# Performance work log

Hardware: AMD Instinct MI355X
Metric: run time of the kernel (lower is better)

## Reference

```python
import jax, jax.numpy as jnp
import numpy as np

N_NODES = 100000
F_IN = 512
HIDDEN = 64
N_CLASS = 40
N_EDGES = 3200000


def gcn_conv(x, src, dst, deg_inv_sqrt, W, b, n_nodes):
    # PyG GCNConv: linear transform, then deg^{-1/2} A_hat deg^{-1/2} aggregation, then bias
    h = x @ W  # [N, out]
    norm = deg_inv_sqrt[src] * deg_inv_sqrt[dst]  # [E+N] (includes self-loops)
    msg = h[src] * norm[:, None]  # gather + scale
    out = jax.ops.segment_sum(msg, dst, num_segments=n_nodes)  # scatter-add
    return out + b


def setup_inputs() -> dict:
    key = jax.random.key(0)
    k1, k2, k3, k4, k5 = jax.random.split(key, 5)
    x = jax.random.normal(k1, (N_NODES, F_IN), dtype=jnp.float32)
    edge_index = jax.random.randint(k2, (2, N_EDGES), 0, N_NODES, dtype=jnp.int64)
    # Glorot-style init for GCN weights
    W1 = jax.random.normal(k3, (F_IN, HIDDEN), dtype=jnp.float32) / np.sqrt(F_IN)
    b1 = jnp.zeros((HIDDEN,), dtype=jnp.float32)
    W2 = jax.random.normal(k4, (HIDDEN, N_CLASS), dtype=jnp.float32) / np.sqrt(HIDDEN)
    b2 = jnp.zeros((N_CLASS,), dtype=jnp.float32)
    return {"x": x, "edge_index": edge_index, "W1": W1, "b1": b1, "W2": W2, "b2": b2}


def reference(x, edge_index, W1, b1, W2, b2):
    n = x.shape[0]
    loops = jnp.arange(n, dtype=edge_index.dtype)
    src = jnp.concatenate([edge_index[0], loops])  # add self-loops (GCNConv default)
    dst = jnp.concatenate([edge_index[1], loops])
    deg = jax.ops.segment_sum(jnp.ones_like(dst, dtype=x.dtype), dst, num_segments=n)
    deg_inv_sqrt = jnp.where(deg > 0, jax.lax.rsqrt(deg), 0.0)
    h = gcn_conv(x, src, dst, deg_inv_sqrt, W1, b1, n)
    h = jax.nn.relu(h)  # dropout treated as eval-mode identity
    x_out = gcn_conv(h, src, dst, deg_inv_sqrt, W2, b2, n)
    return jax.nn.log_softmax(x_out, axis=1), x_out
```

## Files before the change

### kernel.cpp

```cpp
#include <hip/hip_runtime.h>
#include <math.h>

#define N_NODES 100000
#define F_IN    512
#define HIDDEN  64
#define N_CLASS 40
#define N_EDGES 3200000
#define NB      782
#define CAP     6144
#define EPB     8192
#define NPB     391

typedef int EIdx;

typedef __attribute__((ext_vector_type(8))) short short8;
typedef __attribute__((ext_vector_type(4))) float f32x4;
typedef __attribute__((ext_vector_type(4))) unsigned uint4v;

__device__ inline short f2bf(float f) {
    unsigned u = __builtin_bit_cast(unsigned, f);
    unsigned r = u + 0x7FFFu + ((u >> 16) & 1u);
    return (short)(r >> 16);
}

__device__ inline unsigned cvtpk(float lo, float hi) {
    unsigned r;
    asm("v_cvt_pk_bf16_f32 %0, %1, %2" : "=v"(r) : "v"(lo), "v"(hi));
    return r;
}

__device__ inline float bflo(unsigned w) { return __builtin_bit_cast(float, w << 16); }
__device__ inline float bfhi(unsigned w) { return __builtin_bit_cast(float, w & 0xFFFF0000u); }

__global__ __launch_bounds__(256) void binit_kernel(int* __restrict__ bcur) {
    int i = blockIdx.x * 256 + threadIdx.x;
    if (i < NB) bcur[i] = i * CAP;
}

__global__ __launch_bounds__(256) void part1_kernel(const EIdx* __restrict__ src,
                                                    const EIdx* __restrict__ dst,
                                                    int* __restrict__ bcur,
                                                    unsigned* __restrict__ bpacked) {
    __shared__ int hist[NB];
    __shared__ int excl[NB];
    __shared__ int cur[NB];
    __shared__ int delta[NB];
    __shared__ int stmp[256];
    __shared__ unsigned spk[EPB];
    __shared__ unsigned short bid[EPB];
    int t = threadIdx.x;
    int e0 = blockIdx.x * EPB;
    int dreg[32];
    for (int j = t; j < NB; j += 256) hist[j] = 0;
    __syncthreads();
#pragma unroll
    for (int k = 0; k < 32; ++k) {
        int e = e0 + k * 256 + t;
        dreg[k] = (e < N_EDGES) ? dst[e] : -1;
        if (dreg[k] >= 0) atomicAdd(&hist[dreg[k] >> 7], 1);
    }
    __syncthreads();
    {
        int i0 = 4 * t;
        int v0 = (i0 < NB) ? hist[i0] : 0;
        int v1 = (i0 + 1 < NB) ? hist[i0 + 1] : 0;
        int v2 = (i0 + 2 < NB) ? hist[i0 + 2] : 0;
        int v3 = (i0 + 3 < NB) ? hist[i0 + 3] : 0;
        int s = v0 + v1 + v2 + v3;
        stmp[t] = s;
        __syncthreads();
        for (int o = 1; o < 256; o <<= 1) {
            int a = (t >= o) ? stmp[t - o] : 0;
            __syncthreads();
            stmp[t] += a;
            __syncthreads();
        }
        int E = stmp[t] - s;
        if (i0 < NB) excl[i0] = E;
        if (i0 + 1 < NB) excl[i0 + 1] = E + v0;
        if (i0 + 2 < NB) excl[i0 + 2] = E + v0 + v1;
        if (i0 + 3 < NB) excl[i0 + 3] = E + v0 + v1 + v2;
    }
    __syncthreads();
    for (int j = t; j < NB; j += 256) {
        int h = hist[j];
        int rsv = h ? atomicAdd(&bcur[j], h) : 0;
        delta[j] = rsv - excl[j];
        cur[j] = excl[j];
    }
    __syncthreads();
#pragma unroll
    for (int k = 0; k < 32; ++k) {
        int d = dreg[k];
        if (d >= 0) {
            int e = e0 + k * 256 + t;
            int s = src[e];
            int b = d >> 7;
            int p = atomicAdd(&cur[b], 1);
            spk[p] = ((unsigned)(d & 127) << 20) | (unsigned)s;
            bid[p] = (unsigned short)b;
        }
    }
    __syncthreads();
    int cnt = N_EDGES - e0;
    if (cnt > EPB) cnt = EPB;
    for (int i = t; i < cnt; i += 256) {
        int bb = bid[i];
        int pos = i + delta[bb];
        if (pos < (bb + 1) * CAP) bpacked[pos] = spk[i];
    }
}

__global__ __launch_bounds__(256) void part2_kernel(const int* __restrict__ bcur,
                                                    const unsigned* __restrict__ bpacked,
                                                    int* __restrict__ csr_src,
                                                    unsigned* __restrict__ rowmeta,
                                                    float* __restrict__ dis) {
    __shared__ unsigned ent[CAP];
    __shared__ int hist[128];
    __shared__ int stmp[128];
    __shared__ int cur[128];
    int t = threadIdx.x;
    int bk = blockIdx.x;
    int base = bk * CAP;
    int cnt = bcur[bk] - base;
    if (cnt > CAP) cnt = CAP;
    if (t < 128) hist[t] = 0;
    __syncthreads();
    for (int i = t; i < cnt; i += 256) {
        unsigned p = bpacked[base + i];
        ent[i] = p;
        atomicAdd(&hist[p >> 20], 1);
    }
    __syncthreads();
    if (t < 128) stmp[t] = hist[t];
    __syncthreads();
    for (int o = 1; o < 128; o <<= 1) {
        int a = (t >= o && t < 128) ? stmp[t - o] : 0;
        __syncthreads();
        if (t < 128) stmp[t] += a;
        __syncthreads();
    }
    if (t < 128) {
        int ex = stmp[t] - hist[t];
        cur[t] = ex;
        int n = (bk << 7) + t;
        if (n < N_NODES) {
            rowmeta[n] = (unsigned)(base + ex) | ((unsigned)hist[t] << 23);
            dis[n] = rsqrtf((float)(hist[t] + 1));
        }
    }
    __syncthreads();
    for (int i = t; i < cnt; i += 256) {
        unsigned p = ent[i];
        int p2 = atomicAdd(&cur[p >> 20], 1);
        csr_src[base + p2] = (int)(p & 0xFFFFFu);
    }
}

__global__ __launch_bounds__(256) void wprep_kernel(const float* __restrict__ W,
                                                    short* __restrict__ Wbf) {
    int idx = blockIdx.x * 256 + threadIdx.x;
    int k = idx >> 6, col = idx & 63;
    Wbf[col * F_IN + (k ^ ((col & 7) << 3))] = f2bf(W[idx]);
}

__global__ __launch_bounds__(256) void gemm1_mfma_kernel(const float* __restrict__ x,
                                                         const short* __restrict__ Wbf,
                                                         const float* __restrict__ dis,
                                                         unsigned* __restrict__ h1b) {
    __shared__ short Wt[HIDDEN * 128];
    __shared__ short xs[128 * 40];
    int tid = threadIdx.x;
    int wave = tid >> 6, lane = tid & 63;
    int r0 = blockIdx.x * 128;
    int wr0 = r0 + wave * 32;
    int lrow = lane & 15;
    int lk = (lane >> 4) * 8;
    int bswz = (lane & 7) << 3;

    f32x4 acc[2][4];
#pragma unroll
    for (int m = 0; m < 2; ++m)
#pragma unroll
        for (int n = 0; n < 4; ++n) acc[m][n] = (f32x4)0.0f;

    int srow = tid >> 3;
    int schunk = tid & 7;
    int grow[4];
#pragma unroll
    for (int i = 0; i < 4; ++i) {
        int r = r0 + srow + i * 32;
        grow[i] = (r < N_NODES) ? r : (N_NODES - 1);
    }

    float4 xr[4];
#pragma unroll
    for (int i = 0; i < 4; ++i)
        xr[i] = *reinterpret_cast<const float4*>(x + (size_t)grow[i] * F_IN + 4 * schunk);

    const short8* Wv = (const short8*)Wbf;
    short8* Lv = (short8*)Wt;

    for (int ks = 0; ks < 16; ++ks) {
        int kg = ks * 32;
        __syncthreads();
#pragma unroll
        for (int i = 0; i < 4; ++i) {
            uint2 u = {cvtpk(xr[i].x, xr[i].y), cvtpk(xr[i].z, xr[i].w)};
            *reinterpret_cast<uint2*>(&xs[(srow + i * 32) * 40 + 4 * schunk]) = u;
        }
        if ((kg & 127) == 0) {
            int q = kg >> 7;
            for (int i = tid; i < 1024; i += 256) {
                int col = i >> 4, kc = i & 15;
                Lv[i] = Wv[col * 64 + q * 16 + kc];
            }
        }
        __syncthreads();
        if (ks < 15) {
            int kn = kg + 32;
#pragma unroll
            for (int i = 0; i < 4; ++i)
                xr[i] = *reinterpret_cast<const float4*>(x + (size_t)grow[i] * F_IN + kn + 4 * schunk);
        }
        int k0loc = kg & 127;
        short8 a0 = *reinterpret_cast<const short8*>(&xs[(wave * 32 + lrow) * 40 + lk]);
        short8 a1 = *reinterpret_cast<const short8*>(&xs[(wave * 32 + 16 + lrow) * 40 + lk]);
        short8 b[4];
#pragma unroll
        for (int n = 0; n < 4; ++n) {
            int c = n * 16 + lrow;
            b[n] = *reinterpret_cast<const short8*>(&Wt[c * 128 + ((k0loc + lk) ^ bswz)]);
        }
#pragma unroll
        for (int n = 0; n < 4; ++n) {
            acc[0][n] = __builtin_amdgcn_mfma_f32_16x16x32_bf16(a0, b[n], acc[0][n], 0, 0, 0);
            acc[1][n] = __builtin_amdgcn_mfma_f32_16x16x32_bf16(a1, b[n], acc[1][n], 0, 0, 0);
        }
    }

    int crow = (lane >> 4) * 4, ccol = lane & 15;
    bool evenc = (ccol & 1) == 0;
#pragma unroll
    for (int m = 0; m < 2; ++m) {
#pragma unroll
        for (int j = 0; j < 4; ++j) {
            int rr = wr0 + m * 16 + crow + j;
            int rs = (rr < N_NODES) ? rr : (N_NODES - 1);
            float ds = dis[rs];
            float v[4], vn[4];
#pragma unroll
            for (int n = 0; n < 4; ++n) v[n] = acc[m][n][j] * ds;
#pragma unroll
            for (int n = 0; n < 4; ++n) vn[n] = __shfl_xor(v[n], 1);
            if (rr < N_NODES && evenc) {
#pragma unroll
                for (int n = 0; n < 4; ++n)
                    h1b[(size_t)rr * 32 + ((n * 16 + ccol) >> 1)] = cvtpk(v[n], vn[n]);
            }
        }
    }
}

__global__ __launch_bounds__(256) void gather1_kernel(const unsigned* __restrict__ h1b,
                                                      const unsigned* __restrict__ rowmeta,
                                                      const int* __restrict__ csr_src,
                                                      const float* __restrict__ dis,
                                                      const float* __restrict__ b1,
                                                      float* __restrict__ out) {
    int tid = threadIdx.x;
    int n = blockIdx.x * 32 + (tid >> 3);
    int l = tid & 7;
    unsigned meta = rowmeta[n];
    int base = (int)(meta & 0x7FFFFFu);
    int deg = (int)(meta >> 23);
    const unsigned* rowp = h1b + 4 * l;
    uint4 v = *reinterpret_cast<const uint4*>(h1b + (size_t)n * 32 + 4 * l);
    float a0 = bflo(v.x), a1 = bfhi(v.x), a2 = bflo(v.y), a3 = bfhi(v.y);
    float a4 = bflo(v.z), a5 = bfhi(v.z), a6 = bflo(v.w), a7 = bfhi(v.w);
    int e = 0;
    for (; e + 3 < deg; e += 4) {
        int s0 = csr_src[base + e],     s1 = csr_src[base + e + 1];
        int s2 = csr_src[base + e + 2], s3 = csr_src[base + e + 3];
        uint4 r0 = *reinterpret_cast<const uint4*>(rowp + (size_t)s0 * 32);
        uint4 r1 = *reinterpret_cast<const uint4*>(rowp + (size_t)s1 * 32);
        uint4 r2 = *reinterpret_cast<const uint4*>(rowp + (size_t)s2 * 32);
        uint4 r3 = *reinterpret_cast<const uint4*>(rowp + (size_t)s3 * 32);
        a0 += (bflo(r0.x) + bflo(r1.x)) + (bflo(r2.x) + bflo(r3.x));
        a1 += (bfhi(r0.x) + bfhi(r1.x)) + (bfhi(r2.x) + bfhi(r3.x));
        a2 += (bflo(r0.y) + bflo(r1.y)) + (bflo(r2.y) + bflo(r3.y));
        a3 += (bfhi(r0.y) + bfhi(r1.y)) + (bfhi(r2.y) + bfhi(r3.y));
        a4 += (bflo(r0.z) + bflo(r1.z)) + (bflo(r2.z) + bflo(r3.z));
        a5 += (bfhi(r0.z) + bfhi(r1.z)) + (bfhi(r2.z) + bfhi(r3.z));
        a6 += (bflo(r0.w) + bflo(r1.w)) + (bflo(r2.w) + bflo(r3.w));
        a7 += (bfhi(r0.w) + bfhi(r1.w)) + (bfhi(r2.w) + bfhi(r3.w));
    }
    for (; e < deg; ++e) {
        int s = csr_src[base + e];
        uint4 r = *reinterpret_cast<const uint4*>(rowp + (size_t)s * 32);
        a0 += bflo(r.x); a1 += bfhi(r.x); a2 += bflo(r.y); a3 += bfhi(r.y);
        a4 += bflo(r.z); a5 += bfhi(r.z); a6 += bflo(r.w); a7 += bfhi(r.w);
    }
    float ds = dis[n];
    float4 bL = *reinterpret_cast<const float4*>(b1 + 8 * l);
    float4 bH = *reinterpret_cast<const float4*>(b1 + 8 * l + 4);
    float4 oL = {fmaxf(fmaf(a0, ds, bL.x), 0.f), fmaxf(fmaf(a1, ds, bL.y), 0.f),
                 fmaxf(fmaf(a2, ds, bL.z), 0.f), fmaxf(fmaf(a3, ds, bL.w), 0.f)};
    float4 oH = {fmaxf(fmaf(a4, ds, bH.x), 0.f), fmaxf(fmaf(a5, ds, bH.y), 0.f),
                 fmaxf(fmaf(a6, ds, bH.z), 0.f), fmaxf(fmaf(a7, ds, bH.w), 0.f)};
    float* op = out + (size_t)n * HIDDEN + 8 * l;
    *reinterpret_cast<float4*>(op) = oL;
    *reinterpret_cast<float4*>(op + 4) = oH;
}

__global__ __launch_bounds__(256) void gemm2_kernel(const float* __restrict__ x,
                                                    const float* __restrict__ W,
                                                    const float* __restrict__ dis,
                                                    unsigned* __restrict__ h2b) {
    int r = blockIdx.x * 256 + threadIdx.x;
    if (r >= N_NODES) return;
    float acc[N_CLASS];
#pragma unroll
    for (int j = 0; j < N_CLASS; ++j) acc[j] = 0.0f;
    const float* xr = x + (size_t)r * HIDDEN;
    for (int k0 = 0; k0 < HIDDEN; k0 += 4) {
        float4 xv = *reinterpret_cast<const float4*>(xr + k0);
        const float* wk = W + (size_t)k0 * N_CLASS;
#pragma unroll
        for (int j = 0; j < N_CLASS; ++j) {
            acc[j] = fmaf(xv.x, wk[j], acc[j]);
            acc[j] = fmaf(xv.y, wk[N_CLASS + j], acc[j]);
            acc[j] = fmaf(xv.z, wk[2 * N_CLASS + j], acc[j]);
            acc[j] = fmaf(xv.w, wk[3 * N_CLASS + j], acc[j]);
        }
    }
    float ds = dis[r];
    unsigned* hr = h2b + (size_t)r * 20;
#pragma unroll
    for (int q = 0; q < 5; ++q) {
        uint4v o = {cvtpk(acc[8 * q] * ds,     acc[8 * q + 1] * ds),
                    cvtpk(acc[8 * q + 2] * ds, acc[8 * q + 3] * ds),
                    cvtpk(acc[8 * q + 4] * ds, acc[8 * q + 5] * ds),
                    cvtpk(acc[8 * q + 6] * ds, acc[8 * q + 7] * ds)};
        *reinterpret_cast<uint4v*>(hr + 4 * q) = o;
    }
}

__global__ __launch_bounds__(256) void gather2_kernel(const unsigned* __restrict__ h2b,
                                                      const unsigned* __restrict__ rowmeta,
                                                      const int* __restrict__ csr_src,
                                                      const float* __restrict__ dis,
                                                      const float* __restrict__ b2,
                                                      float* __restrict__ xout,
                                                      float* __restrict__ out_ls) {
    int tid = threadIdx.x;
    int n = blockIdx.x * 32 + (tid >> 3);
    int l = tid & 7;
    bool act = l < 5;
    unsigned meta = rowmeta[n];
    int base = (int)(meta & 0x7FFFFFu);
    int deg = (int)(meta >> 23);
    const unsigned* rowp = h2b + 4 * l;
    float a0 = 0.f, a1 = 0.f, a2 = 0.f, a3 = 0.f, a4 = 0.f, a5 = 0.f, a6 = 0.f, a7 = 0.f;
    if (act) {
        uint4 v = *reinterpret_cast<const uint4*>(h2b + (size_t)n * 20 + 4 * l);
        a0 = bflo(v.x); a1 = bfhi(v.x); a2 = bflo(v.y); a3 = bfhi(v.y);
        a4 = bflo(v.z); a5 = bfhi(v.z); a6 = bflo(v.w); a7 = bfhi(v.w);
    }
    int e = 0;
    for (; e + 3 < deg; e += 4) {
        int s0 = csr_src[base + e],     s1 = csr_src[base + e + 1];
        int s2 = csr_src[base + e + 2], s3 = csr_src[base + e + 3];
        if (act) {
            uint4 r0 = *reinterpret_cast<const uint4*>(rowp + (size_t)s0 * 20);
            uint4 r1 = *reinterpret_cast<const uint4*>(rowp + (size_t)s1 * 20);
            uint4 r2 = *reinterpret_cast<const uint4*>(rowp + (size_t)s2 * 20);
            uint4 r3 = *reinterpret_cast<const uint4*>(rowp + (size_t)s3 * 20);
            a0 += (bflo(r0.x) + bflo(r1.x)) + (bflo(r2.x) + bflo(r3.x));
            a1 += (bfhi(r0.x) + bfhi(r1.x)) + (bfhi(r2.x) + bfhi(r3.x));
            a2 += (bflo(r0.y) + bflo(r1.y)) + (bflo(r2.y) + bflo(r3.y));
            a3 += (bfhi(r0.y) + bfhi(r1.y)) + (bfhi(r2.y) + bfhi(r3.y));
            a4 += (bflo(r0.z) + bflo(r1.z)) + (bflo(r2.z) + bflo(r3.z));
            a5 += (bfhi(r0.z) + bfhi(r1.z)) + (bfhi(r2.z) + bfhi(r3.z));
            a6 += (bflo(r0.w) + bflo(r1.w)) + (bflo(r2.w) + bflo(r3.w));
            a7 += (bfhi(r0.w) + bfhi(r1.w)) + (bfhi(r2.w) + bfhi(r3.w));
        }
    }
    for (; e < deg; ++e) {
        int s = csr_src[base + e];
        if (act) {
            uint4 r = *reinterpret_cast<const uint4*>(rowp + (size_t)s * 20);
            a0 += bflo(r.x); a1 += bfhi(r.x); a2 += bflo(r.y); a3 += bfhi(r.y);
            a4 += bflo(r.z); a5 += bfhi(r.z); a6 += bflo(r.w); a7 += bfhi(r.w);
        }
    }
    float ds = dis[n];
    float v0 = 0.f, v1 = 0.f, v2 = 0.f, v3 = 0.f, v4 = 0.f, v5 = 0.f, v6 = 0.f, v7 = 0.f;
    if (act) {
        float4 bL = *reinterpret_cast<const float4*>(b2 + 8 * l);
        float4 bH = *reinterpret_cast<const float4*>(b2 + 8 * l + 4);
        v0 = fmaf(a0, ds, bL.x); v1 = fmaf(a1, ds, bL.y);
        v2 = fmaf(a2, ds, bL.z); v3 = fmaf(a3, ds, bL.w);
        v4 = fmaf(a4, ds, bH.x); v5 = fmaf(a5, ds, bH.y);
        v6 = fmaf(a6, ds, bH.z); v7 = fmaf(a7, ds, bH.w);
    }
    float mx = act ? fmaxf(fmaxf(fmaxf(v0, v1), fmaxf(v2, v3)),
                           fmaxf(fmaxf(v4, v5), fmaxf(v6, v7))) : -INFINITY;
    mx = fmaxf(mx, __shfl_xor(mx, 1));
    mx = fmaxf(mx, __shfl_xor(mx, 2));
    mx = fmaxf(mx, __shfl_xor(mx, 4));
    float sum = act ? ((expf(v0 - mx) + expf(v1 - mx)) + (expf(v2 - mx) + expf(v3 - mx))) +
                      ((expf(v4 - mx) + expf(v5 - mx)) + (expf(v6 - mx) + expf(v7 - mx))) : 0.f;
    sum += __shfl_xor(sum, 1);
    sum += __shfl_xor(sum, 2);
    sum += __shfl_xor(sum, 4);
    if (act) {
        float ls = mx + logf(sum);
        float* xp = xout + (size_t)n * N_CLASS + 8 * l;
        float* lp = out_ls + (size_t)n * N_CLASS + 8 * l;
        float4 xoL = {v0, v1, v2, v3};
        float4 xoH = {v4, v5, v6, v7};
        float4 loL = {v0 - ls, v1 - ls, v2 - ls, v3 - ls};
        float4 loH = {v4 - ls, v5 - ls, v6 - ls, v7 - ls};
        *reinterpret_cast<float4*>(xp) = xoL;
        *reinterpret_cast<float4*>(xp + 4) = xoH;
        *reinterpret_cast<float4*>(lp) = loL;
        *reinterpret_cast<float4*>(lp + 4) = loH;
    }
}

extern "C" void kernel_launch(void* const* d_in, const int* in_sizes, int n_in,
                              void* d_out, int out_size, void* d_ws, size_t ws_size,
                              hipStream_t stream) {
    const float* x  = (const float*)d_in[0];
    const EIdx*  ei = (const EIdx*)d_in[1];
    const float* W1 = (const float*)d_in[2];
    const float* b1 = (const float*)d_in[3];
    const float* W2 = (const float*)d_in[4];
    const float* b2 = (const float*)d_in[5];
    const EIdx* src = ei;
    const EIdx* dst = ei + N_EDGES;

    float* out_ls = (float*)d_out;
    float* x_out  = out_ls + (size_t)N_NODES * N_CLASS;

    char* w = (char*)d_ws;
    int*      bcur    = (int*)w;       w += 1024 * 4;
    float*    dis     = (float*)w;     w += 100352 * 4;
    unsigned* rowmeta = (unsigned*)w;  w += 100352 * 4;
    short*    Wbf     = (short*)w;     w += (size_t)F_IN * HIDDEN * 2;
    unsigned* bpacked = (unsigned*)w;
    unsigned* h1b     = (unsigned*)w;  w += (size_t)NB * CAP * 4;
    int*      csr_src = (int*)w;       w += (size_t)NB * CAP * 4;
    unsigned* h2b     = (unsigned*)w;  w += (size_t)N_NODES * 20 * 4;
    float*    agg1    = (float*)w;     w += (size_t)N_NODES * HIDDEN * 4;

    const int B = 256;
    int gG  = N_NODES / 32;
    int gN  = (N_NODES + B - 1) / B;
    int gM1 = (N_NODES + 127) / 128;

    binit_kernel<<<4, B, 0, stream>>>(bcur);
    part1_kernel<<<NPB, B, 0, stream>>>(src, dst, bcur, bpacked);
    part2_kernel<<<NB, B, 0, stream>>>(bcur, bpacked, csr_src, rowmeta, dis);
    wprep_kernel<<<(F_IN * HIDDEN) / B, B, 0, stream>>>(W1, Wbf);

    gemm1_mfma_kernel<<<gM1, B, 0, stream>>>(x, Wbf, dis, h1b);
    gather1_kernel<<<gG, B, 0, stream>>>(h1b, rowmeta, csr_src, dis, b1, agg1);

    gemm2_kernel<<<gN, B, 0, stream>>>(agg1, W2, dis, h2b);
    gather2_kernel<<<gG, B, 0, stream>>>(h2b, rowmeta, csr_src, dis, b2, x_out, out_ls);
}
```

Before: 273.5 us.

## Merge bucket init into wprep, split LDS histograms, widen gemm1 K-step

Measured after the change: 271.8 us. Within noise of the previous version (-0.6%).

```diff
diff --git a/kernel.cpp b/kernel.cpp
--- a/kernel.cpp
+++ b/kernel.cpp
@@ -32,40 +32,45 @@
 __device__ inline float bflo(unsigned w) { return __builtin_bit_cast(float, w << 16); }
 __device__ inline float bfhi(unsigned w) { return __builtin_bit_cast(float, w & 0xFFFF0000u); }
 
-__global__ __launch_bounds__(256) void binit_kernel(int* __restrict__ bcur) {
-    int i = blockIdx.x * 256 + threadIdx.x;
-    if (i < NB) bcur[i] = i * CAP;
+__global__ __launch_bounds__(256) void wprep_kernel(const float* __restrict__ W,
+                                                    short* __restrict__ Wbf,
+                                                    int* __restrict__ bcur) {
+    int idx = blockIdx.x * 256 + threadIdx.x;
+    if (idx < NB) bcur[idx] = idx * CAP;
+    int k = idx >> 6, col = idx & 63;
+    Wbf[col * F_IN + (k ^ ((col & 7) << 3))] = f2bf(W[idx]);
 }
 
 __global__ __launch_bounds__(256) void part1_kernel(const EIdx* __restrict__ src,
                                                     const EIdx* __restrict__ dst,
                                                     int* __restrict__ bcur,
                                                     unsigned* __restrict__ bpacked) {
-    __shared__ int hist[NB];
+    __shared__ int hist[2 * NB];
     __shared__ int excl[NB];
-    __shared__ int cur[NB];
+    __shared__ int cur[2 * NB];
     __shared__ int delta[NB];
     __shared__ int stmp[256];
     __shared__ unsigned spk[EPB];
     __shared__ unsigned short bid[EPB];
     int t = threadIdx.x;
+    int sub = t >> 7;
     int e0 = blockIdx.x * EPB;
     int dreg[32];
-    for (int j = t; j < NB; j += 256) hist[j] = 0;
+    for (int j = t; j < 2 * NB; j += 256) hist[j] = 0;
     __syncthreads();
 #pragma unroll
     for (int k = 0; k < 32; ++k) {
         int e = e0 + k * 256 + t;
         dreg[k] = (e < N_EDGES) ? dst[e] : -1;
-        if (dreg[k] >= 0) atomicAdd(&hist[dreg[k] >> 7], 1);
+        if (dreg[k] >= 0) atomicAdd(&hist[sub * NB + (dreg[k] >> 7)], 1);
     }
     __syncthreads();
     {
         int i0 = 4 * t;
-        int v0 = (i0 < NB) ? hist[i0] : 0;
-        int v1 = (i0 + 1 < NB) ? hist[i0 + 1] : 0;
-        int v2 = (i0 + 2 < NB) ? hist[i0 + 2] : 0;
-        int v3 = (i0 + 3 < NB) ? hist[i0 + 3] : 0;
+        int v0 = (i0 < NB) ? hist[i0] + hist[NB + i0] : 0;
+        int v1 = (i0 + 1 < NB) ? hist[i0 + 1] + hist[NB + i0 + 1] : 0;
+        int v2 = (i0 + 2 < NB) ? hist[i0 + 2] + hist[NB + i0 + 2] : 0;
+        int v3 = (i0 + 3 < NB) ? hist[i0 + 3] + hist[NB + i0 + 3] : 0;
         int s = v0 + v1 + v2 + v3;
         stmp[t] = s;
         __syncthreads();
@@ -83,10 +88,12 @@
     }
     __syncthreads();
     for (int j = t; j < NB; j += 256) {
-        int h = hist[j];
-        int rsv = h ? atomicAdd(&bcur[j], h) : 0;
+        int h0 = hist[j], h1 = hist[NB + j];
+        int tot = h0 + h1;
+        int rsv = tot ? atomicAdd(&bcur[j], tot) : 0;
         delta[j] = rsv - excl[j];
         cur[j] = excl[j];
+        cur[NB + j] = excl[j] + h0;
     }
     __syncthreads();
 #pragma unroll
@@ -96,7 +103,7 @@
             int e = e0 + k * 256 + t;
             int s = src[e];
             int b = d >> 7;
-            int p = atomicAdd(&cur[b], 1);
+            int p = atomicAdd(&cur[sub * NB + b], 1);
             spk[p] = ((unsigned)(d & 127) << 20) | (unsigned)s;
             bid[p] = (unsigned short)b;
         }
@@ -117,23 +124,24 @@
                                                     unsigned* __restrict__ rowmeta,
                                                     float* __restrict__ dis) {
     __shared__ unsigned ent[CAP];
-    __shared__ int hist[128];
+    __shared__ int hist[2 * 128];
     __shared__ int stmp[128];
-    __shared__ int cur[128];
+    __shared__ int cur[2 * 128];
     int t = threadIdx.x;
+    int sub = t >> 7;
     int bk = blockIdx.x;
     int base = bk * CAP;
     int cnt = bcur[bk] - base;
     if (cnt > CAP) cnt = CAP;
-    if (t < 128) hist[t] = 0;
+    hist[t] = 0;
     __syncthreads();
     for (int i = t; i < cnt; i += 256) {
         unsigned p = bpacked[base + i];
         ent[i] = p;
-        atomicAdd(&hist[p >> 20], 1);
-    }
-    __syncthreads();
-    if (t < 128) stmp[t] = hist[t];
+        atomicAdd(&hist[sub * 128 + (p >> 20)], 1);
+    }
+    __syncthreads();
+    if (t < 128) stmp[t] = hist[t] + hist[128 + t];
     __syncthreads();
     for (int o = 1; o < 128; o <<= 1) {
         int a = (t >= o && t < 128) ? stmp[t - o] : 0;
@@ -142,27 +150,22 @@
         __syncthreads();
     }
     if (t < 128) {
-        int ex = stmp[t] - hist[t];
+        int tot = hist[t] + hist[128 + t];
+        int ex = stmp[t] - tot;
         cur[t] = ex;
+        cur[128 + t] = ex + hist[t];
         int n = (bk << 7) + t;
         if (n < N_NODES) {
-            rowmeta[n] = (unsigned)(base + ex) | ((unsigned)hist[t] << 23);
-            dis[n] = rsqrtf((float)(hist[t] + 1));
+            rowmeta[n] = (unsigned)(base + ex) | ((unsigned)tot << 23);
+            dis[n] = rsqrtf((float)(tot + 1));
         }
     }
     __syncthreads();
     for (int i = t; i < cnt; i += 256) {
         unsigned p = ent[i];
-        int p2 = atomicAdd(&cur[p >> 20], 1);
+        int p2 = atomicAdd(&cur[sub * 128 + (p >> 20)], 1);
         csr_src[base + p2] = (int)(p & 0xFFFFFu);
     }
-}
-
-__global__ __launch_bounds__(256) void wprep_kernel(const float* __restrict__ W,
-                                                    short* __restrict__ Wbf) {
-    int idx = blockIdx.x * 256 + threadIdx.x;
-    int k = idx >> 6, col = idx & 63;
-    Wbf[col * F_IN + (k ^ ((col & 7) << 3))] = f2bf(W[idx]);
 }
 
 __global__ __launch_bounds__(256) void gemm1_mfma_kernel(const float* __restrict__ x,
@@ -170,7 +173,7 @@
                                                          const float* __restrict__ dis,
                                                          unsigned* __restrict__ h1b) {
     __shared__ short Wt[HIDDEN * 128];
-    __shared__ short xs[128 * 40];
+    __shared__ short xs[128 * 72];
     int tid = threadIdx.x;
     int wave = tid >> 6, lane = tid & 63;
     int r0 = blockIdx.x * 128;
@@ -185,58 +188,62 @@
 #pragma unroll
         for (int n = 0; n < 4; ++n) acc[m][n] = (f32x4)0.0f;
 
-    int srow = tid >> 3;
-    int schunk = tid & 7;
-    int grow[4];
-#pragma unroll
-    for (int i = 0; i < 4; ++i) {
-        int r = r0 + srow + i * 32;
+    int srow = tid >> 4;
+    int schunk = tid & 15;
+    int grow[8];
+#pragma unroll
+    for (int i = 0; i < 8; ++i) {
+        int r = r0 + srow + i * 16;
         grow[i] = (r < N_NODES) ? r : (N_NODES - 1);
     }
 
-    float4 xr[4];
-#pragma unroll
-    for (int i = 0; i < 4; ++i)
+    float4 xr[8];
+#pragma unroll
+    for (int i = 0; i < 8; ++i)
         xr[i] = *reinterpret_cast<const float4*>(x + (size_t)grow[i] * F_IN + 4 * schunk);
 
     const short8* Wv = (const short8*)Wbf;
     short8* Lv = (short8*)Wt;
 
-    for (int ks = 0; ks < 16; ++ks) {
-        int kg = ks * 32;
+    for (int ks = 0; ks < 8; ++ks) {
+        int kg = ks * 64;
         __syncthreads();
 #pragma unroll
-        for (int i = 0; i < 4; ++i) {
+        for (int i = 0; i < 8; ++i) {
             uint2 u = {cvtpk(xr[i].x, xr[i].y), cvtpk(xr[i].z, xr[i].w)};
-            *reinterpret_cast<uint2*>(&xs[(srow + i * 32) * 40 + 4 * schunk]) = u;
-        }
-        if ((kg & 127) == 0) {
-            int q = kg >> 7;
+            *reinterpret_cast<uint2*>(&xs[(srow + i * 16) * 72 + 4 * schunk]) = u;
+        }
+        if ((ks & 1) == 0) {
+            int q = ks >> 1;
             for (int i = tid; i < 1024; i += 256) {
                 int col = i >> 4, kc = i & 15;
                 Lv[i] = Wv[col * 64 + q * 16 + kc];
             }
         }
         __syncthreads();
-        if (ks < 15) {
-            int kn = kg + 32;
-#pragma unroll
-            for (int i = 0; i < 4; ++i)
+        if (ks < 7) {
+            int kn = kg + 64;
+#pragma unroll
+            for (int i = 0; i < 8; ++i)
                 xr[i] = *reinterpret_cast<const float4*>(x + (size_t)grow[i] * F_IN + kn + 4 * schunk);
         }
-        int k0loc = kg & 127;
-        short8 a0 = *reinterpret_cast<const short8*>(&xs[(wave * 32 + lrow) * 40 + lk]);
-        short8 a1 = *reinterpret_cast<const short8*>(&xs[(wave * 32 + 16 + lrow) * 40 + lk]);
-        short8 b[4];
-#pragma unroll
-        for (int n = 0; n < 4; ++n) {
-            int c = n * 16 + lrow;
-            b[n] = *reinterpret_cast<const short8*>(&Wt[c * 128 + ((k0loc + lk) ^ bswz)]);
-        }
-#pragma unroll
-        for (int n = 0; n < 4; ++n) {
-            acc[0][n] = __builtin_amdgcn_mfma_f32_16x16x32_bf16(a0, b[n], acc[0][n], 0, 0, 0);
-            acc[1][n] = __builtin_amdgcn_mfma_f32_16x16x32_bf16(a1, b[n], acc[1][n], 0, 0, 0);
+#pragma unroll
+        for (int s = 0; s < 2; ++s) {
+            int kwq = (ks & 1) * 64 + s * 32;
+            int kloc = s * 32;
+            short8 a0 = *reinterpret_cast<const short8*>(&xs[(wave * 32 + lrow) * 72 + kloc + lk]);
+            short8 a1 = *reinterpret_cast<const short8*>(&xs[(wave * 32 + 16 + lrow) * 72 + kloc + lk]);
+            short8 b[4];
+#pragma unroll
+            for (int n = 0; n < 4; ++n) {
+                int c = n * 16 + lrow;
+                b[n] = *reinterpret_cast<const short8*>(&Wt[c * 128 + ((kwq + lk) ^ bswz)]);
+            }
+#pragma unroll
+            for (int n = 0; n < 4; ++n) {
+                acc[0][n] = __builtin_amdgcn_mfma_f32_16x16x32_bf16(a0, b[n], acc[0][n], 0, 0, 0);
+                acc[1][n] = __builtin_amdgcn_mfma_f32_16x16x32_bf16(a1, b[n], acc[1][n], 0, 0, 0);
+            }
         }
     }
 
@@ -461,10 +468,9 @@
     int gN  = (N_NODES + B - 1) / B;
     int gM1 = (N_NODES + 127) / 128;
 
-    binit_kernel<<<4, B, 0, stream>>>(bcur);
+    wprep_kernel<<<(F_IN * HIDDEN) / B, B, 0, stream>>>(W1, Wbf, bcur);
     part1_kernel<<<NPB, B, 0, stream>>>(src, dst, bcur, bpacked);
     part2_kernel<<<NB, B, 0, stream>>>(bcur, bpacked, csr_src, rowmeta, dis);
-    wprep_kernel<<<(F_IN * HIDDEN) / B, B, 0, stream>>>(W1, Wbf);
 
     gemm1_mfma_kernel<<<gM1, B, 0, stream>>>(x, Wbf, dis, h1b);
     gather1_kernel<<<gG, B, 0, stream>>>(h1b, rowmeta, csr_src, dis, b1, agg1);
```
